# Kernel tuning notes

Measured on AMD Instinct MI355X. Metric: run time of the kernel, lower is better.

## Reference

```python
import jax, jax.numpy as jnp
import numpy as np

D_MODEL = 768
N_HEADS = 12
HEAD_DIM = D_MODEL // N_HEADS
B, T = 2, 2048


def setup_inputs() -> dict:
    key = jax.random.key(0)
    k1, k2, k3 = jax.random.split(key, 3)
    x = jax.random.normal(k1, (B, T, D_MODEL), dtype=jnp.float32)
    # causal mask: positions where mask == 0 (False) get -inf
    mask = jnp.tril(jnp.ones((T, T), dtype=bool))[None, None, :, :]
    Wqkv = jax.random.normal(k2, (D_MODEL, 3 * D_MODEL), dtype=jnp.float32) * (D_MODEL ** -0.5)
    bqkv = jnp.zeros((3 * D_MODEL,), dtype=jnp.float32)
    Wout = jax.random.normal(k3, (D_MODEL, D_MODEL), dtype=jnp.float32) * (D_MODEL ** -0.5)
    bout = jnp.zeros((D_MODEL,), dtype=jnp.float32)
    return {"x": x, "mask": mask, "Wqkv": Wqkv, "bqkv": bqkv, "Wout": Wout, "bout": bout}


def reference(x, mask, Wqkv, bqkv, Wout, bout):
    b, t, c = x.shape
    qkv = x @ Wqkv + bqkv                      # [B, T, 3C]
    q, k, v = jnp.split(qkv, 3, axis=-1)
    def heads(z):  # [B, T, C] -> [B, H, T, Dh]
        return z.reshape(b, t, N_HEADS, HEAD_DIM).transpose(0, 2, 1, 3)
    q, k, v = heads(q), heads(k), heads(v)
    scores = jnp.einsum('bhqd,bhkd->bhqk', q, k) / jnp.sqrt(jnp.float32(HEAD_DIM))
    scores = jnp.where(mask, scores, -jnp.inf)
    attn = jax.nn.softmax(scores, axis=-1)
    out = jnp.einsum('bhqk,bhkd->bhqd', attn, v)  # [B, H, T, Dh]
    out = out.transpose(0, 2, 1, 3).reshape(b, t, c)
    # dropout is identity in eval mode
    return out @ Wout + bout
```

## Files before the change

kernel.cpp:

```cpp
#include <hip/hip_runtime.h>
#include <math.h>

#define BB 2
#define TT 2048
#define CC 768
#define HH 12
#define DD 64
#define MROWS (BB*TT)
#define NQKV (3*CC)
#define QBLK 64

typedef short bf16x8 __attribute__((ext_vector_type(8)));
typedef float f32x4 __attribute__((ext_vector_type(4)));

__device__ __forceinline__ unsigned short f2bf(float f) {
    union { float f; unsigned u; } v; v.f = f;
    unsigned u = v.u + 0x7FFF + ((v.u >> 16) & 1);
    return (unsigned short)(u >> 16);
}

__device__ __forceinline__ unsigned cvtpk_bf16(float lo, float hi) {
    unsigned r;
    asm("v_cvt_pk_bf16_f32 %0, %1, %2" : "=v"(r) : "v"(lo), "v"(hi));
    return r;
}

__device__ __forceinline__ void gload_lds16(const void* g, void* l) {
    __builtin_amdgcn_global_load_lds(
        (const __attribute__((address_space(1))) unsigned int*)g,
        (__attribute__((address_space(3))) unsigned int*)l, 16, 0, 0);
}

#define XBLOCKS 512
#define TQKV_TILES ((NQKV/64)*(CC/64))
#define TOUT_TILES ((CC/64)*(CC/64))

__global__ __launch_bounds__(256) void prep(const float* __restrict__ x,
                                            const float* __restrict__ Wqkv,
                                            const float* __restrict__ Wout,
                                            unsigned short* __restrict__ xb,
                                            unsigned short* __restrict__ wqkv_t,
                                            unsigned short* __restrict__ wout_t)
{
    int bid = blockIdx.x;
    if (bid < XBLOCKS) {
        const int total8 = MROWS * CC / 8;
        for (int i = bid * 256 + threadIdx.x; i < total8; i += XBLOCKS * 256) {
            float4 a = ((const float4*)x)[i * 2];
            float4 b = ((const float4*)x)[i * 2 + 1];
            ushort4 lo = { f2bf(a.x), f2bf(a.y), f2bf(a.z), f2bf(a.w) };
            ushort4 hi = { f2bf(b.x), f2bf(b.y), f2bf(b.z), f2bf(b.w) };
            ((ushort4*)xb)[i * 2]     = lo;
            ((ushort4*)xb)[i * 2 + 1] = hi;
        }
        return;
    }
    bid -= XBLOCKS;
    const float* src; unsigned short* dst; int srcN, nt, kt;
    if (bid < TQKV_TILES) { src = Wqkv; dst = wqkv_t; srcN = NQKV;
                            nt = bid % (NQKV/64); kt = bid / (NQKV/64); }
    else { bid -= TQKV_TILES; src = Wout; dst = wout_t; srcN = CC;
           nt = bid % (CC/64); kt = bid / (CC/64); }

    __shared__ float Ts[64][65];
    const int n0 = nt * 64, k0 = kt * 64;
#pragma unroll
    for (int p = 0; p < 4; ++p) {
        int c = p * 256 + threadIdx.x;
        int row = c >> 4, col4 = c & 15;
        float4 v = *(const float4*)&src[(size_t)(k0 + row) * srcN + n0 + col4 * 4];
        Ts[row][col4 * 4 + 0] = v.x;
        Ts[row][col4 * 4 + 1] = v.y;
        Ts[row][col4 * 4 + 2] = v.z;
        Ts[row][col4 * 4 + 3] = v.w;
    }
    __syncthreads();
#pragma unroll
    for (int p = 0; p < 4; ++p) {
        int t = p * 256 + threadIdx.x;
        int on = t >> 4, oslot = t & 15;
        ushort4 o = { f2bf(Ts[oslot * 4 + 0][on]), f2bf(Ts[oslot * 4 + 1][on]),
                      f2bf(Ts[oslot * 4 + 2][on]), f2bf(Ts[oslot * 4 + 3][on]) };
        *(ushort4*)&dst[(size_t)(n0 + on) * CC + k0 + oslot * 4] = o;
    }
}

__global__ __launch_bounds__(256) void qkv_mfma(const unsigned short* __restrict__ A,
                                                const unsigned short* __restrict__ Bt,
                                                const float* __restrict__ bias,
                                                unsigned short* __restrict__ qb,
                                                unsigned short* __restrict__ kb,
                                                unsigned short* __restrict__ vb)
{
    __shared__ unsigned short As[128 * 64];
    __shared__ unsigned short Bs[128 * 64];
    const int tid = threadIdx.x;
    const int wv = tid >> 6, l = tid & 63, g = l >> 4, lr = l & 15;
    const int wm = wv >> 1, wn = wv & 1;
    const int m0 = blockIdx.y * 128, n0 = blockIdx.x * 128;

    f32x4 acc[4][4] = {};

    for (int k0 = 0; k0 < CC; k0 += 64) {
        __syncthreads();
#pragma unroll
        for (int p = 0; p < 4; ++p) {
            int c = p * 256 + tid;
            int row = c >> 3, slot = c & 7;
            gload_lds16(A  + (size_t)(m0 + row) * CC + k0 + slot * 8, As + c * 8);
            gload_lds16(Bt + (size_t)(n0 + row) * CC + k0 + slot * 8, Bs + c * 8);
        }
        __syncthreads();
        bf16x8 af[4][2], bfr[4][2];
#pragma unroll
        for (int i = 0; i < 4; ++i)
#pragma unroll
            for (int kt = 0; kt < 2; ++kt) {
                af[i][kt]  = *(const bf16x8*)&As[(wm * 64 + i * 16 + lr) * 64 + kt * 32 + g * 8];
                bfr[i][kt] = *(const bf16x8*)&Bs[(wn * 64 + i * 16 + lr) * 64 + kt * 32 + g * 8];
            }
#pragma unroll
        for (int i = 0; i < 4; ++i)
#pragma unroll
            for (int j = 0; j < 4; ++j)
#pragma unroll
                for (int kt = 0; kt < 2; ++kt)
                    acc[i][j] = __builtin_amdgcn_mfma_f32_16x16x32_bf16(af[i][kt], bfr[j][kt], acc[i][j], 0, 0, 0);
    }

#pragma unroll
    for (int i = 0; i < 4; ++i)
#pragma unroll
        for (int r = 0; r < 4; ++r) {
            int m = m0 + wm * 64 + i * 16 + 4 * g + r;
            int b_ = m >> 11, t = m & (TT - 1);
#pragma unroll
            for (int j = 0; j < 4; ++j) {
                int n = n0 + wn * 64 + j * 16 + lr;
                float val = acc[i][j][r] + bias[n];
                int which = n / CC;
                int rr = n - which * CC;
                int h = rr >> 6, d = rr & 63;
                size_t bh = (size_t)b_ * HH + h;
                if (which == 0)      qb[(bh * TT + t) * DD + d] = f2bf(val * 0.18033688f);
                else if (which == 1) kb[(bh * TT + t) * DD + d] = f2bf(val);
                else                 vb[(bh * DD + d) * TT + t] = f2bf(val);
            }
        }
}

__global__ __launch_bounds__(256) void out_mfma(const unsigned short* __restrict__ A,
                                                const unsigned short* __restrict__ Bt,
                                                const float* __restrict__ bias,
                                                float* __restrict__ out)
{
    __shared__ unsigned short As[128 * 64];
    __shared__ unsigned short Bs[128 * 64];
    const int tid = threadIdx.x;
    const int wv = tid >> 6, l = tid & 63, g = l >> 4, lr = l & 15;
    const int wm = wv >> 1, wn = wv & 1;
    const int m0 = blockIdx.y * 128, n0 = blockIdx.x * 128;

    f32x4 acc[4][4] = {};

    for (int k0 = 0; k0 < CC; k0 += 64) {
        __syncthreads();
#pragma unroll
        for (int p = 0; p < 4; ++p) {
            int c = p * 256 + tid;
            int row = c >> 3, slot = c & 7;
            gload_lds16(A  + (size_t)(m0 + row) * CC + k0 + slot * 8, As + c * 8);
            gload_lds16(Bt + (size_t)(n0 + row) * CC + k0 + slot * 8, Bs + c * 8);
        }
        __syncthreads();
        bf16x8 af[4][2], bfr[4][2];
#pragma unroll
        for (int i = 0; i < 4; ++i)
#pragma unroll
            for (int kt = 0; kt < 2; ++kt) {
                af[i][kt]  = *(const bf16x8*)&As[(wm * 64 + i * 16 + lr) * 64 + kt * 32 + g * 8];
                bfr[i][kt] = *(const bf16x8*)&Bs[(wn * 64 + i * 16 + lr) * 64 + kt * 32 + g * 8];
            }
#pragma unroll
        for (int i = 0; i < 4; ++i)
#pragma unroll
            for (int j = 0; j < 4; ++j)
#pragma unroll
                for (int kt = 0; kt < 2; ++kt)
                    acc[i][j] = __builtin_amdgcn_mfma_f32_16x16x32_bf16(af[i][kt], bfr[j][kt], acc[i][j], 0, 0, 0);
    }

#pragma unroll
    for (int i = 0; i < 4; ++i)
#pragma unroll
        for (int r = 0; r < 4; ++r) {
            int m = m0 + wm * 64 + i * 16 + 4 * g + r;
#pragma unroll
            for (int j = 0; j < 4; ++j) {
                int n = n0 + wn * 64 + j * 16 + lr;
                out[(size_t)m * CC + n] = acc[i][j][r] + bias[n];
            }
        }
}

__global__ __launch_bounds__(256) void attn_mfma(
    const unsigned short* __restrict__ qb,
    const unsigned short* __restrict__ kb,
    const unsigned short* __restrict__ vtb,
    unsigned short* __restrict__ outp)
{
    __shared__ unsigned short Ks[64 * 64];
    __shared__ unsigned short Vts[64 * 64];

    const int blk  = blockIdx.x;
    const int head = blk % (BB * HH);
    const int qt   = (TT / QBLK - 1) - blk / (BB * HH);
    const int tid  = threadIdx.x;
    const int wv   = tid >> 6;
    const int l    = tid & 63;
    const int g    = l >> 4;
    const int lr   = l & 15;

    const size_t hb = (size_t)head * TT * DD;
    const int qrow0 = qt * QBLK + wv * 16;

    bf16x8 qf[2];
#pragma unroll
    for (int dt = 0; dt < 2; ++dt)
        qf[dt] = *(const bf16x8*)(qb + hb + (size_t)(qrow0 + lr) * DD + dt * 32 + 8 * g);

    f32x4 oacc[4] = {};
    float lpart = 0.f;

    const int srow0 = tid >> 3, srow1 = srow0 + 32;
    const int slot  = tid & 7;
#define RHO(k) ((((k) >> 5) << 5) | ((((k) >> 2) & 1) << 4) | ((((k) >> 3) & 3) << 2) | ((k) & 3))
    const int rho0 = RHO(srow0), rho1 = RHO(srow1);
    const int koff0 = (rho0 * 64 + slot * 8) ^ ((rho0 & 7) << 3);
    const int koff1 = (rho1 * 64 + slot * 8) ^ ((rho1 & 7) << 3);
    const int voff0 = (srow0 * 64 + slot * 8) ^ ((srow0 & 7) << 3);
    const int voff1 = (srow1 * 64 + slot * 8) ^ ((srow1 & 7) << 3);
    const unsigned short* kg0 = kb  + hb + (size_t)srow0 * DD + slot * 8;
    const unsigned short* kg1 = kb  + hb + (size_t)srow1 * DD + slot * 8;
    const unsigned short* vg0 = vtb + hb + (size_t)srow0 * TT + slot * 8;
    const unsigned short* vg1 = vtb + hb + (size_t)srow1 * TT + slot * 8;

    for (int c = 0; c <= qt; ++c) {
        __syncthreads();
        *(bf16x8*)&Ks[koff0]  = *(const bf16x8*)(kg0 + (size_t)c * 64 * DD);
        *(bf16x8*)&Ks[koff1]  = *(const bf16x8*)(kg1 + (size_t)c * 64 * DD);
        *(bf16x8*)&Vts[voff0] = *(const bf16x8*)(vg0 + c * 64);
        *(bf16x8*)&Vts[voff1] = *(const bf16x8*)(vg1 + c * 64);
        __syncthreads();

        f32x4 sacc[4] = {};
#pragma unroll
        for (int jt = 0; jt < 4; ++jt) {
#pragma unroll
            for (int dt = 0; dt < 2; ++dt) {
                int prow = jt * 16 + lr;
                int off = (prow * 64 + dt * 32 + g * 8) ^ ((prow & 7) << 3);
                bf16x8 kf = *(const bf16x8*)&Ks[off];
                sacc[jt] = __builtin_amdgcn_mfma_f32_16x16x32_bf16(kf, qf[dt], sacc[jt], 0, 0, 0);
            }
        }

        float pv[4][4];
        const int qloc = wv * 16 + lr;
        const bool diag = (c == qt);
#pragma unroll
        for (int jt = 0; jt < 4; ++jt)
#pragma unroll
            for (int r = 0; r < 4; ++r) {
                float p = __builtin_amdgcn_exp2f(sacc[jt][r]);
                if (diag) {
                    int keyl = 32 * (jt >> 1) + 8 * g + 4 * (jt & 1) + r;
                    if (keyl > qloc) p = 0.f;
                }
                pv[jt][r] = p;
                lpart += p;
            }

        union { bf16x8 v; unsigned u[4]; } pf0, pf1;
        pf0.u[0] = cvtpk_bf16(pv[0][0], pv[0][1]);
        pf0.u[1] = cvtpk_bf16(pv[0][2], pv[0][3]);
        pf0.u[2] = cvtpk_bf16(pv[1][0], pv[1][1]);
        pf0.u[3] = cvtpk_bf16(pv[1][2], pv[1][3]);
        pf1.u[0] = cvtpk_bf16(pv[2][0], pv[2][1]);
        pf1.u[1] = cvtpk_bf16(pv[2][2], pv[2][3]);
        pf1.u[2] = cvtpk_bf16(pv[3][0], pv[3][1]);
        pf1.u[3] = cvtpk_bf16(pv[3][2], pv[3][3]);

#pragma unroll
        for (int dt = 0; dt < 4; ++dt) {
#pragma unroll
            for (int kt = 0; kt < 2; ++kt) {
                int row = dt * 16 + lr;
                int off = (row * 64 + kt * 32 + g * 8) ^ ((row & 7) << 3);
                bf16x8 vf = *(const bf16x8*)&Vts[off];
                oacc[dt] = __builtin_amdgcn_mfma_f32_16x16x32_bf16(
                    kt ? pf1.v : pf0.v, vf, oacc[dt], 0, 0, 0);
            }
        }
    }

    float lsum = lpart;
    lsum += __shfl_xor(lsum, 16);
    lsum += __shfl_xor(lsum, 32);
    float linv[4];
#pragma unroll
    for (int r = 0; r < 4; ++r)
        linv[r] = 1.f / __shfl(lsum, 4 * g + r);

    const int b_ = head / HH, h = head % HH;
#pragma unroll
    for (int dt = 0; dt < 4; ++dt)
#pragma unroll
        for (int r = 0; r < 4; ++r) {
            int qg = qrow0 + 4 * g + r;
            outp[((size_t)b_ * TT + qg) * CC + h * DD + dt * 16 + lr] =
                f2bf(oacc[dt][r] * linv[r]);
        }
}

extern "C" void kernel_launch(void* const* d_in, const int* in_sizes, int n_in,
                              void* d_out, int out_size, void* d_ws, size_t ws_size,
                              hipStream_t stream)
{
    const float* x    = (const float*)d_in[0];
    const float* Wqkv = (const float*)d_in[2];
    const float* bqkv = (const float*)d_in[3];
    const float* Wout = (const float*)d_in[4];
    const float* bout = (const float*)d_in[5];
    float* out = (float*)d_out;

    unsigned short* p = (unsigned short*)d_ws;
    unsigned short* xb      = p;  p += (size_t)MROWS * CC;
    unsigned short* wqkv_t  = p;  p += (size_t)NQKV * CC;
    unsigned short* wout_t  = p;  p += (size_t)CC * CC;
    unsigned short* qb      = p;  p += (size_t)BB * HH * TT * DD;
    unsigned short* kb      = p;  p += (size_t)BB * HH * TT * DD;
    unsigned short* vb      = p;  p += (size_t)BB * HH * TT * DD;
    unsigned short* attnb   = p;  p += (size_t)MROWS * CC;

    prep<<<XBLOCKS + TQKV_TILES + TOUT_TILES, 256, 0, stream>>>(x, Wqkv, Wout, xb, wqkv_t, wout_t);

    dim3 g1(NQKV / 128, MROWS / 128);
    qkv_mfma<<<g1, 256, 0, stream>>>(xb, wqkv_t, bqkv, qb, kb, vb);

    dim3 g2(BB * HH * (TT / QBLK));
    attn_mfma<<<g2, 256, 0, stream>>>(qb, kb, vb, attnb);

    dim3 g3(CC / 128, MROWS / 128);
    out_mfma<<<g3, 256, 0, stream>>>(attnb, wout_t, bout, out);
}
```

Before: 191.6 us.

## Double-buffer K/V tiles in attention and shrink GEMM M-tiles to 64

The attention kernel now prefetches the next K/V chunk into registers while computing on the current chunk, then writes it into a second LDS buffer. This removes one barrier per iteration and hides global-load latency. MFMA sections are wrapped in s_setprio to favour matrix issue. The QKV and output projection GEMMs use 64-row tiles instead of 128, doubling the block count for better CU occupancy, at the cost of less data reuse per block and more register pressure from the prefetch.

```diff
diff --git a/kernel.cpp b/kernel.cpp
--- a/kernel.cpp
+++ b/kernel.cpp
@@ -92,35 +92,43 @@
                                                 unsigned short* __restrict__ kb,
                                                 unsigned short* __restrict__ vb)
 {
-    __shared__ unsigned short As[128 * 64];
+    __shared__ unsigned short As[64 * 64];
     __shared__ unsigned short Bs[128 * 64];
     const int tid = threadIdx.x;
     const int wv = tid >> 6, l = tid & 63, g = l >> 4, lr = l & 15;
     const int wm = wv >> 1, wn = wv & 1;
-    const int m0 = blockIdx.y * 128, n0 = blockIdx.x * 128;
-
-    f32x4 acc[4][4] = {};
+    const int m0 = blockIdx.y * 64, n0 = blockIdx.x * 128;
+
+    f32x4 acc[2][4] = {};
 
     for (int k0 = 0; k0 < CC; k0 += 64) {
         __syncthreads();
+#pragma unroll
+        for (int p = 0; p < 2; ++p) {
+            int c = p * 256 + tid;
+            int row = c >> 3, slot = c & 7;
+            gload_lds16(A + (size_t)(m0 + row) * CC + k0 + slot * 8, As + c * 8);
+        }
 #pragma unroll
         for (int p = 0; p < 4; ++p) {
             int c = p * 256 + tid;
             int row = c >> 3, slot = c & 7;
-            gload_lds16(A  + (size_t)(m0 + row) * CC + k0 + slot * 8, As + c * 8);
             gload_lds16(Bt + (size_t)(n0 + row) * CC + k0 + slot * 8, Bs + c * 8);
         }
         __syncthreads();
-        bf16x8 af[4][2], bfr[4][2];
-#pragma unroll
-        for (int i = 0; i < 4; ++i)
-#pragma unroll
-            for (int kt = 0; kt < 2; ++kt) {
-                af[i][kt]  = *(const bf16x8*)&As[(wm * 64 + i * 16 + lr) * 64 + kt * 32 + g * 8];
-                bfr[i][kt] = *(const bf16x8*)&Bs[(wn * 64 + i * 16 + lr) * 64 + kt * 32 + g * 8];
-            }
-#pragma unroll
-        for (int i = 0; i < 4; ++i)
+        bf16x8 af[2][2], bfr[4][2];
+#pragma unroll
+        for (int i = 0; i < 2; ++i)
+#pragma unroll
+            for (int kt = 0; kt < 2; ++kt)
+                af[i][kt] = *(const bf16x8*)&As[(wm * 32 + i * 16 + lr) * 64 + kt * 32 + g * 8];
+#pragma unroll
+        for (int j = 0; j < 4; ++j)
+#pragma unroll
+            for (int kt = 0; kt < 2; ++kt)
+                bfr[j][kt] = *(const bf16x8*)&Bs[(wn * 64 + j * 16 + lr) * 64 + kt * 32 + g * 8];
+#pragma unroll
+        for (int i = 0; i < 2; ++i)
 #pragma unroll
             for (int j = 0; j < 4; ++j)
 #pragma unroll
@@ -129,10 +137,10 @@
     }
 
 #pragma unroll
-    for (int i = 0; i < 4; ++i)
+    for (int i = 0; i < 2; ++i)
 #pragma unroll
         for (int r = 0; r < 4; ++r) {
-            int m = m0 + wm * 64 + i * 16 + 4 * g + r;
+            int m = m0 + wm * 32 + i * 16 + 4 * g + r;
             int b_ = m >> 11, t = m & (TT - 1);
 #pragma unroll
             for (int j = 0; j < 4; ++j) {
@@ -154,35 +162,43 @@
                                                 const float* __restrict__ bias,
                                                 float* __restrict__ out)
 {
-    __shared__ unsigned short As[128 * 64];
+    __shared__ unsigned short As[64 * 64];
     __shared__ unsigned short Bs[128 * 64];
     const int tid = threadIdx.x;
     const int wv = tid >> 6, l = tid & 63, g = l >> 4, lr = l & 15;
     const int wm = wv >> 1, wn = wv & 1;
-    const int m0 = blockIdx.y * 128, n0 = blockIdx.x * 128;
-
-    f32x4 acc[4][4] = {};
+    const int m0 = blockIdx.y * 64, n0 = blockIdx.x * 128;
+
+    f32x4 acc[2][4] = {};
 
     for (int k0 = 0; k0 < CC; k0 += 64) {
         __syncthreads();
+#pragma unroll
+        for (int p = 0; p < 2; ++p) {
+            int c = p * 256 + tid;
+            int row = c >> 3, slot = c & 7;
+            gload_lds16(A + (size_t)(m0 + row) * CC + k0 + slot * 8, As + c * 8);
+        }
 #pragma unroll
         for (int p = 0; p < 4; ++p) {
             int c = p * 256 + tid;
             int row = c >> 3, slot = c & 7;
-            gload_lds16(A  + (size_t)(m0 + row) * CC + k0 + slot * 8, As + c * 8);
             gload_lds16(Bt + (size_t)(n0 + row) * CC + k0 + slot * 8, Bs + c * 8);
         }
         __syncthreads();
-        bf16x8 af[4][2], bfr[4][2];
-#pragma unroll
-        for (int i = 0; i < 4; ++i)
-#pragma unroll
-            for (int kt = 0; kt < 2; ++kt) {
-                af[i][kt]  = *(const bf16x8*)&As[(wm * 64 + i * 16 + lr) * 64 + kt * 32 + g * 8];
-                bfr[i][kt] = *(const bf16x8*)&Bs[(wn * 64 + i * 16 + lr) * 64 + kt * 32 + g * 8];
-            }
-#pragma unroll
-        for (int i = 0; i < 4; ++i)
+        bf16x8 af[2][2], bfr[4][2];
+#pragma unroll
+        for (int i = 0; i < 2; ++i)
+#pragma unroll
+            for (int kt = 0; kt < 2; ++kt)
+                af[i][kt] = *(const bf16x8*)&As[(wm * 32 + i * 16 + lr) * 64 + kt * 32 + g * 8];
+#pragma unroll
+        for (int j = 0; j < 4; ++j)
+#pragma unroll
+            for (int kt = 0; kt < 2; ++kt)
+                bfr[j][kt] = *(const bf16x8*)&Bs[(wn * 64 + j * 16 + lr) * 64 + kt * 32 + g * 8];
+#pragma unroll
+        for (int i = 0; i < 2; ++i)
 #pragma unroll
             for (int j = 0; j < 4; ++j)
 #pragma unroll
@@ -191,10 +207,10 @@
     }
 
 #pragma unroll
-    for (int i = 0; i < 4; ++i)
+    for (int i = 0; i < 2; ++i)
 #pragma unroll
         for (int r = 0; r < 4; ++r) {
-            int m = m0 + wm * 64 + i * 16 + 4 * g + r;
+            int m = m0 + wm * 32 + i * 16 + 4 * g + r;
 #pragma unroll
             for (int j = 0; j < 4; ++j) {
                 int n = n0 + wn * 64 + j * 16 + lr;
@@ -209,8 +225,8 @@
     const unsigned short* __restrict__ vtb,
     unsigned short* __restrict__ outp)
 {
-    __shared__ unsigned short Ks[64 * 64];
-    __shared__ unsigned short Vts[64 * 64];
+    __shared__ unsigned short Ks[2 * 64 * 64];
+    __shared__ unsigned short Vts[2 * 64 * 64];
 
     const int blk  = blockIdx.x;
     const int head = blk % (BB * HH);
@@ -245,25 +261,36 @@
     const unsigned short* vg0 = vtb + hb + (size_t)srow0 * TT + slot * 8;
     const unsigned short* vg1 = vtb + hb + (size_t)srow1 * TT + slot * 8;
 
+    *(bf16x8*)&Ks[koff0]  = *(const bf16x8*)(kg0);
+    *(bf16x8*)&Ks[koff1]  = *(const bf16x8*)(kg1);
+    *(bf16x8*)&Vts[voff0] = *(const bf16x8*)(vg0);
+    *(bf16x8*)&Vts[voff1] = *(const bf16x8*)(vg1);
+    __syncthreads();
+
+    int bo = 0;
     for (int c = 0; c <= qt; ++c) {
-        __syncthreads();
-        *(bf16x8*)&Ks[koff0]  = *(const bf16x8*)(kg0 + (size_t)c * 64 * DD);
-        *(bf16x8*)&Ks[koff1]  = *(const bf16x8*)(kg1 + (size_t)c * 64 * DD);
-        *(bf16x8*)&Vts[voff0] = *(const bf16x8*)(vg0 + c * 64);
-        *(bf16x8*)&Vts[voff1] = *(const bf16x8*)(vg1 + c * 64);
-        __syncthreads();
+        const bool more = (c < qt);
+        bf16x8 nk0, nk1, nv0, nv1;
+        if (more) {
+            nk0 = *(const bf16x8*)(kg0 + (size_t)(c + 1) * 64 * DD);
+            nk1 = *(const bf16x8*)(kg1 + (size_t)(c + 1) * 64 * DD);
+            nv0 = *(const bf16x8*)(vg0 + (c + 1) * 64);
+            nv1 = *(const bf16x8*)(vg1 + (c + 1) * 64);
+        }
 
         f32x4 sacc[4] = {};
+        __builtin_amdgcn_s_setprio(1);
 #pragma unroll
         for (int jt = 0; jt < 4; ++jt) {
 #pragma unroll
             for (int dt = 0; dt < 2; ++dt) {
                 int prow = jt * 16 + lr;
-                int off = (prow * 64 + dt * 32 + g * 8) ^ ((prow & 7) << 3);
+                int off = bo + ((prow * 64 + dt * 32 + g * 8) ^ ((prow & 7) << 3));
                 bf16x8 kf = *(const bf16x8*)&Ks[off];
                 sacc[jt] = __builtin_amdgcn_mfma_f32_16x16x32_bf16(kf, qf[dt], sacc[jt], 0, 0, 0);
             }
         }
+        __builtin_amdgcn_s_setprio(0);
 
         float pv[4][4];
         const int qloc = wv * 16 + lr;
@@ -291,16 +318,28 @@
         pf1.u[2] = cvtpk_bf16(pv[3][0], pv[3][1]);
         pf1.u[3] = cvtpk_bf16(pv[3][2], pv[3][3]);
 
+        __builtin_amdgcn_s_setprio(1);
 #pragma unroll
         for (int dt = 0; dt < 4; ++dt) {
 #pragma unroll
             for (int kt = 0; kt < 2; ++kt) {
                 int row = dt * 16 + lr;
-                int off = (row * 64 + kt * 32 + g * 8) ^ ((row & 7) << 3);
+                int off = bo + ((row * 64 + kt * 32 + g * 8) ^ ((row & 7) << 3));
                 bf16x8 vf = *(const bf16x8*)&Vts[off];
                 oacc[dt] = __builtin_amdgcn_mfma_f32_16x16x32_bf16(
                     kt ? pf1.v : pf0.v, vf, oacc[dt], 0, 0, 0);
             }
+        }
+        __builtin_amdgcn_s_setprio(0);
+
+        if (more) {
+            int nb = bo ^ (64 * 64);
+            *(bf16x8*)&Ks[nb + koff0]  = nk0;
+            *(bf16x8*)&Ks[nb + koff1]  = nk1;
+            *(bf16x8*)&Vts[nb + voff0] = nv0;
+            *(bf16x8*)&Vts[nb + voff1] = nv1;
+            __syncthreads();
+            bo = nb;
         }
     }
 
@@ -345,12 +384,12 @@
 
     prep<<<XBLOCKS + TQKV_TILES + TOUT_TILES, 256, 0, stream>>>(x, Wqkv, Wout, xb, wqkv_t, wout_t);
 
-    dim3 g1(NQKV / 128, MROWS / 128);
+    dim3 g1(NQKV / 128, MROWS / 64);
     qkv_mfma<<<g1, 256, 0, stream>>>(xb, wqkv_t, bqkv, qb, kb, vb);
 
     dim3 g2(BB * HH * (TT / QBLK));
     attn_mfma<<<g2, 256, 0, stream>>>(qb, kb, vb, attnb);
 
-    dim3 g3(CC / 128, MROWS / 128);
+    dim3 g3(CC / 128, MROWS / 64);
     out_mfma<<<g3, 256, 0, stream>>>(attnb, wout_t, bout, out);
 }
```

After: 177.5 us. -7.4%, faster.
